# Optimization experiments

Measured on AMD Instinct MI355X. Metric: run time of the kernel, lower is better.

## Reference

```python
import jax, jax.numpy as jnp
import numpy as np

B, T, Q, K = 64, 2048, 512, 512

def setup_inputs() -> dict:
    key0 = jax.random.key(0)
    k1, k2, k3 = jax.random.split(key0, 3)
    query = jax.random.normal(k1, (B, Q), dtype=jnp.float32)
    key = jax.random.normal(k2, (B, T, K), dtype=jnp.float32)
    # learned params: weights ~ U(-0.1, 0.1), bias zeros(1)
    W = jax.random.uniform(k3, (K, Q), dtype=jnp.float32) * 0.2 - 0.1
    bias = jnp.zeros((1,), dtype=jnp.float32)
    return {"query": query, "key": key, "W": W, "bias": bias}

def reference(query, key, W, bias):
    # mids = W @ query : [B, K]
    mids = jnp.einsum('kq,bq->bk', W, query)
    # scores = tanh(key . mids + bias) : [B, T]
    scores = jnp.tanh(jnp.einsum('btk,bk->bt', key, mids) + bias)
    return jax.nn.softmax(scores, axis=1)
```

## Files before the change

kernel.cpp:

```cpp
#include <hip/hip_runtime.h>
#include <math.h>

#define WAVE 64

__global__ void mids_kernel(const float* __restrict__ W,
                            const float* __restrict__ query,
                            float* __restrict__ mids,
                            int B, int K, int Q) {
    int gwave = (int)((blockIdx.x * blockDim.x + threadIdx.x) / WAVE);
    int lane  = threadIdx.x & (WAVE - 1);
    int total = B * K;
    if (gwave >= total) return;
    int b = gwave / K;
    int k = gwave - b * K;

    const float4* wrow = (const float4*)(W + (size_t)k * Q);
    const float4* qrow = (const float4*)(query + (size_t)b * Q);

    float acc = 0.f;
    int nvec = Q >> 2;
    for (int i = lane; i < nvec; i += WAVE) {
        float4 w = wrow[i];
        float4 q = qrow[i];
        acc += w.x * q.x + w.y * q.y + w.z * q.z + w.w * q.w;
    }
    #pragma unroll
    for (int off = 32; off > 0; off >>= 1)
        acc += __shfl_down(acc, off, WAVE);
    if (lane == 0) mids[gwave] = acc;
}

__global__ void scores_kernel(const float* __restrict__ key,
                              const float* __restrict__ mids,
                              const float* __restrict__ bias,
                              float* __restrict__ scores,
                              int B, int T, int K) {
    int gwave = (int)((blockIdx.x * blockDim.x + threadIdx.x) / WAVE);
    int lane  = threadIdx.x & (WAVE - 1);
    int total = B * T;
    if (gwave >= total) return;
    int b = gwave / T;

    const float4* krow = (const float4*)(key  + (size_t)gwave * K);
    const float4* mrow = (const float4*)(mids + (size_t)b * K);

    float acc = 0.f;
    #pragma unroll
    for (int i = 0; i < 2; ++i) {
        int idx = lane + i * WAVE;
        float4 kk = krow[idx];
        float4 mm = mrow[idx];
        acc += kk.x * mm.x + kk.y * mm.y + kk.z * mm.z + kk.w * mm.w;
    }
    #pragma unroll
    for (int off = 32; off > 0; off >>= 1)
        acc += __shfl_down(acc, off, WAVE);
    if (lane == 0) scores[gwave] = tanhf(acc + bias[0]);
}

__global__ void softmax_kernel(float* __restrict__ out, int T) {
    const int b   = blockIdx.x;
    const int tid = threadIdx.x;
    const int lane = tid & (WAVE - 1);
    const int wid  = tid >> 6;
    float* row = out + (size_t)b * T;

    __shared__ float red[4];

    float vals[8];
    float m = -INFINITY;
    #pragma unroll
    for (int i = 0; i < 8; ++i) {
        vals[i] = row[tid + i * 256];
        m = fmaxf(m, vals[i]);
    }
    #pragma unroll
    for (int off = 32; off > 0; off >>= 1)
        m = fmaxf(m, __shfl_down(m, off, WAVE));
    if (lane == 0) red[wid] = m;
    __syncthreads();
    m = fmaxf(fmaxf(red[0], red[1]), fmaxf(red[2], red[3]));
    __syncthreads();

    float s = 0.f;
    #pragma unroll
    for (int i = 0; i < 8; ++i) {
        vals[i] = expf(vals[i] - m);
        s += vals[i];
    }
    #pragma unroll
    for (int off = 32; off > 0; off >>= 1)
        s += __shfl_down(s, off, WAVE);
    if (lane == 0) red[wid] = s;
    __syncthreads();
    s = red[0] + red[1] + red[2] + red[3];

    float inv = 1.f / s;
    #pragma unroll
    for (int i = 0; i < 8; ++i)
        row[tid + i * 256] = vals[i] * inv;
}

extern "C" void kernel_launch(void* const* d_in, const int* in_sizes, int n_in,
                              void* d_out, int out_size, void* d_ws, size_t ws_size,
                              hipStream_t stream) {
    const float* query = (const float*)d_in[0];
    const float* key   = (const float*)d_in[1];
    const float* W     = (const float*)d_in[2];
    const float* bias  = (const float*)d_in[3];
    float* out  = (float*)d_out;
    float* mids = (float*)d_ws;

    const int B = 64, T = 2048, Q = 512, K = 512;

    mids_kernel<<<(B * K) / 4, 256, 0, stream>>>(W, query, mids, B, K, Q);

    scores_kernel<<<(B * T) / 4, 256, 0, stream>>>(key, mids, bias, out, B, T, K);

    softmax_kernel<<<B, 256, 0, stream>>>(out, T);
}
```

Before: 366.1 us.

## Process multiple rows per wave in mids and scores kernels

Each wave in the mids kernel now computes 8 outputs, loading the query row once and reusing it. Each wave in the scores kernel now handles 16 key rows, keeping the mids vector in registers, issuing several independent loads per iteration and writing four tanh results as one float4. Shuffle reductions switch to xor-based butterflies. The aim is to cut redundant mids/query loads and per-wave overhead, and to raise memory-level parallelism on the bandwidth-bound key read, at the cost of more registers per thread and hardcoded dimensions.

```diff
diff --git a/kernel.cpp b/kernel.cpp
--- a/kernel.cpp
+++ b/kernel.cpp
@@ -3,64 +3,95 @@
 
 #define WAVE 64
 
+
 __global__ void mids_kernel(const float* __restrict__ W,
                             const float* __restrict__ query,
-                            float* __restrict__ mids,
-                            int B, int K, int Q) {
-    int gwave = (int)((blockIdx.x * blockDim.x + threadIdx.x) / WAVE);
-    int lane  = threadIdx.x & (WAVE - 1);
-    int total = B * K;
-    if (gwave >= total) return;
-    int b = gwave / K;
-    int k = gwave - b * K;
+                            float* __restrict__ mids) {
+    const int gwave = (int)((blockIdx.x * blockDim.x + threadIdx.x) >> 6);
+    const int lane  = threadIdx.x & 63;
+    const int b  = gwave >> 6;
+    const int k0 = (gwave & 63) * 8;
 
-    const float4* wrow = (const float4*)(W + (size_t)k * Q);
-    const float4* qrow = (const float4*)(query + (size_t)b * Q);
+    const float4* qrow = (const float4*)(query + (size_t)b * 512);
+    const float4 q0 = qrow[lane];
+    const float4 q1 = qrow[lane + 64];
 
-    float acc = 0.f;
-    int nvec = Q >> 2;
-    for (int i = lane; i < nvec; i += WAVE) {
-        float4 w = wrow[i];
-        float4 q = qrow[i];
-        acc += w.x * q.x + w.y * q.y + w.z * q.z + w.w * q.w;
+    float s[8];
+    #pragma unroll
+    for (int r = 0; r < 8; ++r) {
+        const float4* wrow = (const float4*)(W + (size_t)(k0 + r) * 512);
+        float4 a = wrow[lane];
+        float4 c = wrow[lane + 64];
+        s[r] = a.x*q0.x + a.y*q0.y + a.z*q0.z + a.w*q0.w
+             + c.x*q1.x + c.y*q1.y + c.z*q1.z + c.w*q1.w;
     }
     #pragma unroll
-    for (int off = 32; off > 0; off >>= 1)
-        acc += __shfl_down(acc, off, WAVE);
-    if (lane == 0) mids[gwave] = acc;
+    for (int off = 32; off > 0; off >>= 1) {
+        #pragma unroll
+        for (int r = 0; r < 8; ++r)
+            s[r] += __shfl_xor(s[r], off, WAVE);
+    }
+    if (lane == 0) {
+        float4* dst = (float4*)(mids + (size_t)gwave * 8);
+        dst[0] = make_float4(s[0], s[1], s[2], s[3]);
+        dst[1] = make_float4(s[4], s[5], s[6], s[7]);
+    }
 }
 
 __global__ void scores_kernel(const float* __restrict__ key,
                               const float* __restrict__ mids,
                               const float* __restrict__ bias,
-                              float* __restrict__ scores,
-                              int B, int T, int K) {
-    int gwave = (int)((blockIdx.x * blockDim.x + threadIdx.x) / WAVE);
-    int lane  = threadIdx.x & (WAVE - 1);
-    int total = B * T;
-    if (gwave >= total) return;
-    int b = gwave / T;
+                              float* __restrict__ out) {
+    const int gwave = (int)((blockIdx.x * blockDim.x + threadIdx.x) >> 6);
+    const int lane  = threadIdx.x & 63;
+    const int row0  = gwave * 16;
+    const int b     = row0 >> 11;
 
-    const float4* krow = (const float4*)(key  + (size_t)gwave * K);
-    const float4* mrow = (const float4*)(mids + (size_t)b * K);
+    const float4* mrow = (const float4*)(mids + (size_t)b * 512);
+    const float4 m0 = mrow[lane];
+    const float4 m1 = mrow[lane + 64];
+    const float bv = bias[0];
 
-    float acc = 0.f;
+    const float4* kbase = (const float4*)key + (size_t)row0 * 128;
+
     #pragma unroll
-    for (int i = 0; i < 2; ++i) {
-        int idx = lane + i * WAVE;
-        float4 kk = krow[idx];
-        float4 mm = mrow[idx];
-        acc += kk.x * mm.x + kk.y * mm.y + kk.z * mm.z + kk.w * mm.w;
+    for (int r = 0; r < 16; r += 4) {
+        float4 a0 = kbase[(size_t)(r+0)*128 + lane];
+        float4 c0 = kbase[(size_t)(r+0)*128 + lane + 64];
+        float4 a1 = kbase[(size_t)(r+1)*128 + lane];
+        float4 c1 = kbase[(size_t)(r+1)*128 + lane + 64];
+        float4 a2 = kbase[(size_t)(r+2)*128 + lane];
+        float4 c2 = kbase[(size_t)(r+2)*128 + lane + 64];
+        float4 a3 = kbase[(size_t)(r+3)*128 + lane];
+        float4 c3 = kbase[(size_t)(r+3)*128 + lane + 64];
+
+        float s0 = a0.x*m0.x + a0.y*m0.y + a0.z*m0.z + a0.w*m0.w
+                 + c0.x*m1.x + c0.y*m1.y + c0.z*m1.z + c0.w*m1.w;
+        float s1 = a1.x*m0.x + a1.y*m0.y + a1.z*m0.z + a1.w*m0.w
+                 + c1.x*m1.x + c1.y*m1.y + c1.z*m1.z + c1.w*m1.w;
+        float s2 = a2.x*m0.x + a2.y*m0.y + a2.z*m0.z + a2.w*m0.w
+                 + c2.x*m1.x + c2.y*m1.y + c2.z*m1.z + c2.w*m1.w;
+        float s3 = a3.x*m0.x + a3.y*m0.y + a3.z*m0.z + a3.w*m0.w
+                 + c3.x*m1.x + c3.y*m1.y + c3.z*m1.z + c3.w*m1.w;
+
+        #pragma unroll
+        for (int off = 32; off > 0; off >>= 1) {
+            s0 += __shfl_xor(s0, off, WAVE);
+            s1 += __shfl_xor(s1, off, WAVE);
+            s2 += __shfl_xor(s2, off, WAVE);
+            s3 += __shfl_xor(s3, off, WAVE);
+        }
+        if (lane == 0) {
+            *(float4*)(out + (size_t)row0 + r) =
+                make_float4(tanhf(s0 + bv), tanhf(s1 + bv),
+                            tanhf(s2 + bv), tanhf(s3 + bv));
+        }
     }
-    #pragma unroll
-    for (int off = 32; off > 0; off >>= 1)
-        acc += __shfl_down(acc, off, WAVE);
-    if (lane == 0) scores[gwave] = tanhf(acc + bias[0]);
 }
 
 __global__ void softmax_kernel(float* __restrict__ out, int T) {
-    const int b   = blockIdx.x;
-    const int tid = threadIdx.x;
+    const int b    = blockIdx.x;
+    const int tid  = threadIdx.x;
     const int lane = tid & (WAVE - 1);
     const int wid  = tid >> 6;
     float* row = out + (size_t)b * T;
@@ -76,7 +107,7 @@
     }
     #pragma unroll
     for (int off = 32; off > 0; off >>= 1)
-        m = fmaxf(m, __shfl_down(m, off, WAVE));
+        m = fmaxf(m, __shfl_xor(m, off, WAVE));
     if (lane == 0) red[wid] = m;
     __syncthreads();
     m = fmaxf(fmaxf(red[0], red[1]), fmaxf(red[2], red[3]));
@@ -90,7 +121,7 @@
     }
     #pragma unroll
     for (int off = 32; off > 0; off >>= 1)
-        s += __shfl_down(s, off, WAVE);
+        s += __shfl_xor(s, off, WAVE);
     if (lane == 0) red[wid] = s;
     __syncthreads();
     s = red[0] + red[1] + red[2] + red[3];
@@ -111,11 +142,11 @@
     float* out  = (float*)d_out;
     float* mids = (float*)d_ws;
 
-    const int B = 64, T = 2048, Q = 512, K = 512;
+    const int B = 64, T = 2048;
 
-    mids_kernel<<<(B * K) / 4, 256, 0, stream>>>(W, query, mids, B, K, Q);
+    mids_kernel<<<1024, 256, 0, stream>>>(W, query, mids);
 
-    scores_kernel<<<(B * T) / 4, 256, 0, stream>>>(key, mids, bias, out, B, T, K);
+    scores_kernel<<<2048, 256, 0, stream>>>(key, mids, bias, out);
 
     softmax_kernel<<<B, 256, 0, stream>>>(out, T);
 }
```

Result: no change. 371.5 us (+1.5%).
